# Kernel tuning notes

Measured on AMD Instinct MI355X. Metric: run time of the kernel, lower is better.

Reference implementation:

```python
import jax, jax.numpy as jnp
import numpy as np

REG_CONST = 0.05  # matches init_kwargs reg_const


def setup_inputs() -> dict:
    key = jax.random.key(0)
    k1, k2, k3 = jax.random.split(key, 3)
    N, D, C = 1_000_000, 128, 10
    X_train = jax.random.normal(k1, (N, D), dtype=jnp.float32)
    y_train = jax.random.randint(k2, (N,), 0, C)
    w = jax.random.normal(k3, (C, D), dtype=jnp.float32) * 0.01
    return {"X_train": X_train, "y_train": y_train, "w": w}


def reference(X_train, y_train, w):
    """Vectorized SVM.calc_gradient: multiclass hinge loss + gradient w.r.t. w.

    Original loops over samples i and classes c:
      margin = scores[c] - scores[y_i] + 1; if margin > 0 (c != y_i):
        loss += margin; grad[y_i] += X[i]; grad[c] -= X[i]
    then loss /= N (+ 0.5*reg*||w||^2), grad /= N (+ reg*w).
    (The original seeds `gradients` with np.random.rand -- a bug; we use the
    intended zero init so the math is deterministic.)
    """
    N = X_train.shape[0]
    C = w.shape[0]
    inv_n = jnp.asarray(1.0 / N, dtype=X_train.dtype)

    scores = X_train @ w.T                                        # [N, C]
    correct = jnp.take_along_axis(scores, y_train[:, None], axis=1)  # [N, 1]
    margins = scores - correct + 1.0                              # [N, C]
    onehot = jax.nn.one_hot(y_train, C, dtype=scores.dtype)       # [N, C]
    mask = jnp.where((margins > 0) & (onehot == 0), 1.0, 0.0).astype(scores.dtype)

    loss = jnp.sum(mask * margins) * inv_n + 0.5 * REG_CONST * jnp.sum(w * w)

    # grad[c] gets -X[i] for each violating (i, c); grad[y_i] gets +X[i] per
    # violating class -> counts[i] copies of X[i] scatter-added to row y_i.
    counts = mask.sum(axis=1)                                     # [N]
    neg_part = mask.T @ X_train                                   # [C, D]
    pos_part = jax.ops.segment_sum(counts[:, None] * X_train, y_train,
                                   num_segments=C)                # [C, D]
    gradients = (pos_part - neg_part) * inv_n + REG_CONST * w
    return gradients, loss
```

## Files before the change

### kernel.cpp

```cpp
#include <hip/hip_runtime.h>

#define REG_CONST 0.05f
#define NCLASS 10
#define DIM 128
#define TILE 64
#define NBLOCKS 768
#define NTHREADS 256

__device__ __forceinline__ void async_ld16(const void* g, void* l) {
  __builtin_amdgcn_global_load_lds(
      (const __attribute__((address_space(1))) void*)g,
      (__attribute__((address_space(3))) void*)l, 16, 0, 0);
}

__global__ __launch_bounds__(NTHREADS, 3)
void svm_fused(const float* __restrict__ X, const int* __restrict__ y,
               const float* __restrict__ w, float* __restrict__ out,
               int ntiles, float inv_n) {
  __shared__ float4 xs[2048];
  __shared__ float4 coefs[192];
  __shared__ float4 wlds4[360];
  __shared__ float  lred[4];

  float* wlds = (float*)wlds4;
  const int t  = threadIdx.x;
  const int l  = t & 63;
  const int wv = t >> 6;

  for (int i = t; i < NCLASS * DIM; i += NTHREADS) {
    int d = i & 127;
    wlds[(i >> 7) * 144 + d + ((d >> 5) << 2)] = w[i];
  }

  const float4* X4 = (const float4*)X;

  const int p1row = (wv << 4) + (l >> 2);
  const int dq    = l & 3;
  const int d4p2 = t & 31;
  const int rg   = t >> 5;

  float4 g[10];
  #pragma unroll
  for (int c = 0; c < 10; ++c) g[c] = make_float4(0.f, 0.f, 0.f, 0.f);
  float loss_acc = 0.f;

  for (int tix = blockIdx.x; tix < ntiles; tix += gridDim.x) {
    const int row0 = tix * TILE;
    __syncthreads();
    #pragma unroll
    for (int ii = 0; ii < 8; ++ii) {
      int i   = (wv << 3) + ii;
      int row = (i << 1) + (l >> 5);
      int d4  = (l & 31) ^ (row & 31);
      async_ld16(X4 + (size_t)(row0 + row) * 32 + d4, xs + (i << 6) + l);
    }
    __syncthreads();

    float s[10];
    #pragma unroll
    for (int c = 0; c < 10; ++c) s[c] = 0.f;
    #pragma unroll
    for (int j = 0; j < 8; ++j) {
      int d4 = (dq << 3) + j;
      float4 x4 = xs[(p1row << 5) + (d4 ^ (p1row & 31))];
      #pragma unroll
      for (int c = 0; c < 10; ++c) {
        float4 w4 = wlds4[c * 36 + dq * 9 + j];
        s[c] = fmaf(x4.x, w4.x, fmaf(x4.y, w4.y,
               fmaf(x4.z, w4.z, fmaf(x4.w, w4.w, s[c]))));
      }
    }
    #pragma unroll
    for (int c = 0; c < 10; ++c) {
      s[c] += __shfl_xor(s[c], 1);
      s[c] += __shfl_xor(s[c], 2);
    }

    int yv = y[row0 + p1row];
    float sy = s[0];
    #pragma unroll
    for (int c = 1; c < 10; ++c) sy = (c == yv) ? s[c] : sy;

    float cnt = 0.f, rl = 0.f;
    float cf[10];
    #pragma unroll
    for (int c = 0; c < 10; ++c) {
      float m = s[c] - sy + 1.0f;
      bool act = (m > 0.f) && (c != yv);
      cf[c] = act ? -1.f : 0.f;
      cnt += act ? 1.f : 0.f;
      rl  += act ? m : 0.f;
    }
    #pragma unroll
    for (int c = 0; c < 10; ++c) cf[c] = (c == yv) ? cnt : cf[c];
    coefs[p1row * 3 + 0] = make_float4(cf[0], cf[1], cf[2], cf[3]);
    coefs[p1row * 3 + 1] = make_float4(cf[4], cf[5], cf[6], cf[7]);
    coefs[p1row * 3 + 2] = make_float4(cf[8], cf[9], 0.f, 0.f);
    if (dq == 0) loss_acc += rl;
    __syncthreads();

    #pragma unroll
    for (int k = 0; k < 8; ++k) {
      int r = (k << 3) + rg;
      float4 x4 = xs[(r << 5) + (d4p2 ^ (r & 31))];
      float4 c0 = coefs[r * 3 + 0];
      float4 c1 = coefs[r * 3 + 1];
      float4 c2 = coefs[r * 3 + 2];
#define ACC4(cc, gi)                         \
      g[gi].x = fmaf(cc, x4.x, g[gi].x);     \
      g[gi].y = fmaf(cc, x4.y, g[gi].y);     \
      g[gi].z = fmaf(cc, x4.z, g[gi].z);     \
      g[gi].w = fmaf(cc, x4.w, g[gi].w);
      ACC4(c0.x, 0) ACC4(c0.y, 1) ACC4(c0.z, 2) ACC4(c0.w, 3)
      ACC4(c1.x, 4) ACC4(c1.y, 5) ACC4(c1.z, 6) ACC4(c1.w, 7)
      ACC4(c2.x, 8) ACC4(c2.y, 9)
#undef ACC4
    }
  }

  float contrib = loss_acc * inv_n;
  if (blockIdx.x == 0) {
    float rw = 0.f;
    for (int i = t; i < NCLASS * DIM; i += NTHREADS) rw = fmaf(w[i], w[i], rw);
    contrib = fmaf(0.5f * REG_CONST, rw, contrib);
  }
  #pragma unroll
  for (int off = 32; off; off >>= 1) contrib += __shfl_down(contrib, off);
  if (l == 0) lred[wv] = contrib;
  __syncthreads();
  if (t == 0) atomicAdd(out + NCLASS * DIM, lred[0] + lred[1] + lred[2] + lred[3]);

  float4* red = xs;
  #pragma unroll
  for (int chunk = 0; chunk < 2; ++chunk) {
    __syncthreads();
    #pragma unroll
    for (int k = 0; k < 5; ++k) red[k * 256 + t] = g[chunk * 5 + k];
    __syncthreads();
    if (t < 160) {
      int k = t >> 5, dd = t & 31;
      float sx = 0.f, syy = 0.f, sz = 0.f, sw = 0.f;
      #pragma unroll
      for (int r8 = 0; r8 < 8; ++r8) {
        float4 v = red[k * 256 + (r8 << 5) + dd];
        sx += v.x; syy += v.y; sz += v.z; sw += v.w;
      }
      int c = chunk * 5 + k;
      int base = c * DIM + (dd << 2);
      float ax = sx * inv_n, ay = syy * inv_n, az = sz * inv_n, aw = sw * inv_n;
      if (blockIdx.x == 0) {
        ax += REG_CONST * w[base + 0];
        ay += REG_CONST * w[base + 1];
        az += REG_CONST * w[base + 2];
        aw += REG_CONST * w[base + 3];
      }
      atomicAdd(out + base + 0, ax);
      atomicAdd(out + base + 1, ay);
      atomicAdd(out + base + 2, az);
      atomicAdd(out + base + 3, aw);
    }
  }
}

extern "C" void kernel_launch(void* const* d_in, const int* in_sizes, int n_in,
                              void* d_out, int out_size, void* d_ws, size_t ws_size,
                              hipStream_t stream) {
  const float* X = (const float*)d_in[0];
  const int*   y = (const int*)d_in[1];
  const float* w = (const float*)d_in[2];
  float* out = (float*)d_out;
  int N = in_sizes[1];
  int ntiles = N / TILE;
  float inv_n = 1.0f / (float)N;
  hipMemsetAsync(d_out, 0, (size_t)out_size * sizeof(float), stream);
  svm_fused<<<NBLOCKS, NTHREADS, 0, stream>>>(X, y, w, out, ntiles, inv_n);
}
```

Measured before the change: 727.7 us.

## Double-buffer X tiles in LDS and keep w in registers for scoring

The X tile buffer becomes a double buffer, so the async global-to-LDS loads for the next tile are issued while the gradient accumulation of the current tile runs, instead of waiting on each load. The weight matrix moves from LDS into registers: each thread holds two float4 slices per class, and the score computation switches to 16 lanes per row with a 4-step shuffle reduction. Grid size and the occupancy hint drop from 3 to 2 blocks per CU, since the larger LDS footprint and extra registers lower occupancy. The risk is less latency hiding from fewer resident waves and more shuffle work per row.

```diff
diff --git a/kernel.cpp b/kernel.cpp
--- a/kernel.cpp
+++ b/kernel.cpp
@@ -4,7 +4,7 @@
 #define NCLASS 10
 #define DIM 128
 #define TILE 64
-#define NBLOCKS 768
+#define NBLOCKS 512
 #define NTHREADS 256
 
 __device__ __forceinline__ void async_ld16(const void* g, void* l) {
@@ -13,96 +13,120 @@
       (__attribute__((address_space(3))) void*)l, 16, 0, 0);
 }
 
-__global__ __launch_bounds__(NTHREADS, 3)
+__global__ __launch_bounds__(NTHREADS, 2)
 void svm_fused(const float* __restrict__ X, const int* __restrict__ y,
                const float* __restrict__ w, float* __restrict__ out,
                int ntiles, float inv_n) {
-  __shared__ float4 xs[2048];
+  __shared__ float4 xs[2][2048];
   __shared__ float4 coefs[192];
-  __shared__ float4 wlds4[360];
   __shared__ float  lred[4];
 
-  float* wlds = (float*)wlds4;
   const int t  = threadIdx.x;
   const int l  = t & 63;
   const int wv = t >> 6;
 
-  for (int i = t; i < NCLASS * DIM; i += NTHREADS) {
-    int d = i & 127;
-    wlds[(i >> 7) * 144 + d + ((d >> 5) << 2)] = w[i];
+  const int q  = t & 15;
+  const int rp = t >> 4;
+
+  const float4* W4 = (const float4*)w;
+  float4 wr[NCLASS][2];
+  #pragma unroll
+  for (int c = 0; c < NCLASS; ++c) {
+    wr[c][0] = W4[c * 32 + q];
+    wr[c][1] = W4[c * 32 + q + 16];
   }
 
   const float4* X4 = (const float4*)X;
-
-  const int p1row = (wv << 4) + (l >> 2);
-  const int dq    = l & 3;
   const int d4p2 = t & 31;
   const int rg   = t >> 5;
 
-  float4 g[10];
-  #pragma unroll
-  for (int c = 0; c < 10; ++c) g[c] = make_float4(0.f, 0.f, 0.f, 0.f);
+  float4 g[NCLASS];
+  #pragma unroll
+  for (int c = 0; c < NCLASS; ++c) g[c] = make_float4(0.f, 0.f, 0.f, 0.f);
   float loss_acc = 0.f;
 
-  for (int tix = blockIdx.x; tix < ntiles; tix += gridDim.x) {
-    const int row0 = tix * TILE;
-    __syncthreads();
+  {
+    const int nrow0 = blockIdx.x * TILE;
     #pragma unroll
     for (int ii = 0; ii < 8; ++ii) {
       int i   = (wv << 3) + ii;
       int row = (i << 1) + (l >> 5);
       int d4  = (l & 31) ^ (row & 31);
-      async_ld16(X4 + (size_t)(row0 + row) * 32 + d4, xs + (i << 6) + l);
-    }
-    __syncthreads();
-
-    float s[10];
-    #pragma unroll
-    for (int c = 0; c < 10; ++c) s[c] = 0.f;
-    #pragma unroll
-    for (int j = 0; j < 8; ++j) {
-      int d4 = (dq << 3) + j;
-      float4 x4 = xs[(p1row << 5) + (d4 ^ (p1row & 31))];
-      #pragma unroll
-      for (int c = 0; c < 10; ++c) {
-        float4 w4 = wlds4[c * 36 + dq * 9 + j];
-        s[c] = fmaf(x4.x, w4.x, fmaf(x4.y, w4.y,
-               fmaf(x4.z, w4.z, fmaf(x4.w, w4.w, s[c]))));
-      }
-    }
-    #pragma unroll
-    for (int c = 0; c < 10; ++c) {
-      s[c] += __shfl_xor(s[c], 1);
-      s[c] += __shfl_xor(s[c], 2);
-    }
-
-    int yv = y[row0 + p1row];
-    float sy = s[0];
-    #pragma unroll
-    for (int c = 1; c < 10; ++c) sy = (c == yv) ? s[c] : sy;
-
-    float cnt = 0.f, rl = 0.f;
-    float cf[10];
-    #pragma unroll
-    for (int c = 0; c < 10; ++c) {
-      float m = s[c] - sy + 1.0f;
-      bool act = (m > 0.f) && (c != yv);
-      cf[c] = act ? -1.f : 0.f;
-      cnt += act ? 1.f : 0.f;
-      rl  += act ? m : 0.f;
-    }
-    #pragma unroll
-    for (int c = 0; c < 10; ++c) cf[c] = (c == yv) ? cnt : cf[c];
-    coefs[p1row * 3 + 0] = make_float4(cf[0], cf[1], cf[2], cf[3]);
-    coefs[p1row * 3 + 1] = make_float4(cf[4], cf[5], cf[6], cf[7]);
-    coefs[p1row * 3 + 2] = make_float4(cf[8], cf[9], 0.f, 0.f);
-    if (dq == 0) loss_acc += rl;
-    __syncthreads();
+      async_ld16(X4 + (size_t)(nrow0 + row) * 32 + d4, &xs[0][(i << 6) + l]);
+    }
+  }
+
+  int cur = 0;
+  for (int tix = blockIdx.x; tix < ntiles; tix += gridDim.x) {
+    const int row0 = tix * TILE;
+    __syncthreads();
+    const float4* xb = xs[cur];
+
+    #pragma unroll
+    for (int pass = 0; pass < 4; ++pass) {
+      const int row = (pass << 4) + rp;
+      float4 xa = xb[(row << 5) + ( q        ^ (row & 31))];
+      float4 xc = xb[(row << 5) + ((q + 16)  ^ (row & 31))];
+      float s[NCLASS];
+      #pragma unroll
+      for (int c = 0; c < NCLASS; ++c) {
+        float v;
+        v = fmaf(xa.x, wr[c][0].x, fmaf(xa.y, wr[c][0].y,
+            fmaf(xa.z, wr[c][0].z, xa.w * wr[c][0].w)));
+        v = fmaf(xc.x, wr[c][1].x, fmaf(xc.y, wr[c][1].y,
+            fmaf(xc.z, wr[c][1].z, fmaf(xc.w, wr[c][1].w, v))));
+        s[c] = v;
+      }
+      #pragma unroll
+      for (int m = 1; m <= 8; m <<= 1) {
+        #pragma unroll
+        for (int c = 0; c < NCLASS; ++c) s[c] += __shfl_xor(s[c], m);
+      }
+
+      int yv = y[row0 + row];
+      float sy = s[0];
+      #pragma unroll
+      for (int c = 1; c < NCLASS; ++c) sy = (c == yv) ? s[c] : sy;
+
+      float cnt = 0.f, rl = 0.f;
+      float cf[NCLASS];
+      #pragma unroll
+      for (int c = 0; c < NCLASS; ++c) {
+        float mg = s[c] - sy + 1.0f;
+        bool act = (mg > 0.f) && (c != yv);
+        cf[c] = act ? -1.f : 0.f;
+        cnt += act ? 1.f : 0.f;
+        rl  += act ? mg : 0.f;
+      }
+      #pragma unroll
+      for (int c = 0; c < NCLASS; ++c) cf[c] = (c == yv) ? cnt : cf[c];
+
+      if (q == 0) {
+        coefs[row * 3 + 0] = make_float4(cf[0], cf[1], cf[2], cf[3]);
+        coefs[row * 3 + 1] = make_float4(cf[4], cf[5], cf[6], cf[7]);
+        coefs[row * 3 + 2] = make_float4(cf[8], cf[9], 0.f, 0.f);
+        loss_acc += rl;
+      }
+    }
+    __syncthreads();
+
+    int nxt = tix + gridDim.x;
+    if (nxt < ntiles) {
+      const int nrow0 = nxt * TILE;
+      float4* dst = xs[cur ^ 1];
+      #pragma unroll
+      for (int ii = 0; ii < 8; ++ii) {
+        int i   = (wv << 3) + ii;
+        int row = (i << 1) + (l >> 5);
+        int d4  = (l & 31) ^ (row & 31);
+        async_ld16(X4 + (size_t)(nrow0 + row) * 32 + d4, dst + (i << 6) + l);
+      }
+    }
 
     #pragma unroll
     for (int k = 0; k < 8; ++k) {
       int r = (k << 3) + rg;
-      float4 x4 = xs[(r << 5) + (d4p2 ^ (r & 31))];
+      float4 x4 = xb[(r << 5) + (d4p2 ^ (r & 31))];
       float4 c0 = coefs[r * 3 + 0];
       float4 c1 = coefs[r * 3 + 1];
       float4 c2 = coefs[r * 3 + 2];
@@ -116,6 +140,7 @@
       ACC4(c2.x, 8) ACC4(c2.y, 9)
 #undef ACC4
     }
+    cur ^= 1;
   }
 
   float contrib = loss_acc * inv_n;
@@ -130,7 +155,7 @@
   __syncthreads();
   if (t == 0) atomicAdd(out + NCLASS * DIM, lred[0] + lred[1] + lred[2] + lred[3]);
 
-  float4* red = xs;
+  float4* red = (float4*)xs;
   #pragma unroll
   for (int chunk = 0; chunk < 2; ++chunk) {
     __syncthreads();
```

Measured after the change: 960.4 us. +32.0%, slower.
